# Kernel tuning notes

Hardware: AMD Instinct MI355X
Metric: run time of the kernel (lower is better)

## Reference

```python
import jax, jax.numpy as jnp
import numpy as np

M, B, S = 8, 64, 1024
I = K = V = 256
H = 8
F = 1024


def setup_inputs() -> dict:
    key0 = jax.random.key(0)
    ks = iter(jax.random.split(key0, 64))
    nrm = lambda shp, s=1.0: jax.random.normal(next(ks), shp, dtype=jnp.float32) * s
    w = 0.05
    inp = {
        's0': nrm((M, B, I)), 'q0': nrm((M, B, K)), 'k0': nrm((M, B, K)), 'v0': nrm((M, B, V)),
        'key': nrm((S, B, K)), 'value': nrm((S, B, V)),
        'attn_wq': nrm((M, K, K), w), 'attn_wk': nrm((M, K, K), w), 'attn_wv': nrm((M, K, K), w),
        'attn_bq': nrm((M, K), w), 'attn_bk': nrm((M, K), w), 'attn_bv': nrm((M, K), w),
        'attn_wo': nrm((M, K, K), w), 'attn_bo': nrm((M, K), w),
    }
    for p, out in (('q', K), ('k', K), ('v', V), ('s', I)):
        inp[p + '_w1'] = nrm((M, 2 * I, F), w)
        inp[p + '_b1'] = nrm((M, F), w)
        inp[p + '_w2'] = nrm((M, F, out), w)
        inp[p + '_b2'] = nrm((M, out), w)
    inp['g_w1'] = nrm((4, M, 2 * I, F), w)
    inp['g_b1'] = nrm((4, M, F), w)
    inp['g_w2'] = nrm((4, M, F, 1), w)
    inp['g_b2'] = nrm((4, M, 1), w)
    return inp


def _forward(s0, q0, k0, v0, key, value,
             attn_wq, attn_wk, attn_wv, attn_bq, attn_bk, attn_bv, attn_wo, attn_bo,
             q_w1, q_b1, q_w2, q_b2, k_w1, k_b1, k_w2, k_b2,
             v_w1, v_b1, v_w2, v_b2, s_w1, s_b1, s_w2, s_b2,
             g_w1, g_b1, g_w2, g_b2):
    m, b, kd = q0.shape
    s = key.shape[0]
    hd = kd // H
    # per-module projections (single-query decode-style attention)
    q = jnp.einsum('mbk,mkd->mbd', q0, attn_wq) + attn_bq[:, None, :]          # (M,B,K)
    kk = jnp.einsum('sbk,mkd->msbd', key, attn_wk) + attn_bk[:, None, None, :]  # (M,S,B,K)
    vv = jnp.einsum('sbk,mkd->msbd', value, attn_wv) + attn_bv[:, None, None, :]
    qh = q.reshape(m, b, H, hd)
    kh = kk.reshape(m, s, b, H, hd)
    vh = vv.reshape(m, s, b, H, hd)
    scores = jnp.einsum('mbhd,msbhd->mbhs', qh, kh) / jnp.sqrt(jnp.float32(hd))
    aw = jax.nn.softmax(scores, axis=-1)                                        # (M,B,H,S)
    ctx = jnp.einsum('mbhs,msbhd->mbhd', aw, vh).reshape(m, b, kd)
    attn_out = jnp.einsum('mbk,mko->mbo', ctx, attn_wo) + attn_bo[:, None, :]   # (M,B,K)
    attn_weights = aw.mean(axis=2)                                              # (M,B,S)

    # _make_mlp puts ReLU FIRST: Seq(ReLU, Lin, ReLU, Lin, last_act)
    fc_in = jax.nn.relu(jnp.concatenate([attn_out, s0], axis=-1))               # (M,B,2I)

    def head(w1, b1, w2, b2):
        h = jax.nn.relu(jnp.einsum('mbi,mif->mbf', fc_in, w1) + b1[:, None, :])
        return jnp.einsum('mbf,mfo->mbo', h, w2) + b2[:, None, :]

    # non-gate heads: last activation ReLU, then .tanh() in forward
    oq = jnp.tanh(jax.nn.relu(head(q_w1, q_b1, q_w2, q_b2)))
    ok = jnp.tanh(jax.nn.relu(head(k_w1, k_b1, k_w2, k_b2)))
    ov = jnp.tanh(jax.nn.relu(head(v_w1, v_b1, v_w2, v_b2)))
    os_ = jnp.tanh(jax.nn.relu(head(s_w1, s_b1, s_w2, s_b2)))

    # gate heads stacked on leading g axis (query,key,value,state)
    gh = jax.nn.relu(jnp.einsum('mbi,gmif->gmbf', fc_in, g_w1) + g_b1[:, :, None, :])
    gates = jax.nn.sigmoid(jnp.einsum('gmbf,gmfo->gmbo', gh, g_w2) + g_b2[:, :, None, :])
    qg, kg, vg, sg = gates[0], gates[1], gates[2], gates[3]

    gq = qg * oq + (1.0 - qg) * q0
    gk = kg * ok + (1.0 - kg) * k0
    gv = vg * ov + (1.0 - vg) * v0
    gs = sg * os_ + (1.0 - sg) * s0
    return attn_out, attn_weights, gs, gq, gk, gv


def reference(s0, q0, k0, v0, key, value,
              attn_wq, attn_wk, attn_wv, attn_bq, attn_bk, attn_bv, attn_wo, attn_bo,
              q_w1, q_b1, q_w2, q_b2, k_w1, k_b1, k_w2, k_b2,
              v_w1, v_b1, v_w2, v_b2, s_w1, s_b1, s_w2, s_b2,
              g_w1, g_b1, g_w2, g_b2):
    return _forward(s0, q0, k0, v0, key, value,
                    attn_wq, attn_wk, attn_wv, attn_bq, attn_bk, attn_bv, attn_wo, attn_bo,
                    q_w1, q_b1, q_w2, q_b2, k_w1, k_b1, k_w2, k_b2,
                    v_w1, v_b1, v_w2, v_b2, s_w1, s_b1, s_w2, s_b2,
                    g_w1, g_b1, g_w2, g_b2)
```

## Files before the change

kernel.cpp:

```cpp
#include <hip/hip_runtime.h>
#include <math.h>

#define Mm 8
#define Bb 64
#define Ss 1024
#define Kk 256
#define Hh 8
#define HD 32
#define Ff 1024

typedef _Float16 f16x8 __attribute__((ext_vector_type(8)));
typedef float f32x4 __attribute__((ext_vector_type(4)));

#define WS_Q      0u
#define WS_U      131072u
#define WS_QDB    1179648u
#define WS_SC     1183744u
#define WS_W      5378048u
#define WS_H1     6426624u
#define WS_FC     0u
#define WS_GATES  262144u
#define WS_HPART  1183744u

__device__ __forceinline__ unsigned pk2(float a, float b) {
  union { unsigned u; _Float16 h[2]; } c;
  c.h[0] = (_Float16)a; c.h[1] = (_Float16)b;
  return c.u;
}

__global__ __launch_bounds__(256) void k1_qproj(
    const float* __restrict__ q0, const float* __restrict__ wq,
    const float* __restrict__ bq, float* __restrict__ qout) {
  __shared__ float q0s[8 * 260];
  const int m = blockIdx.x, b0 = blockIdx.y * 8, t = threadIdx.x;
#pragma unroll
  for (int j = 0; j < 8; ++j)
    q0s[j * 260 + t] = q0[(m * Bb + b0 + j) * Kk + t];
  __syncthreads();
  float acc[8];
  const float bias = bq[m * Kk + t];
#pragma unroll
  for (int j = 0; j < 8; ++j) acc[j] = bias;
  const float* wcol = wq + m * Kk * Kk + t;
  for (int k4 = 0; k4 < Kk / 4; ++k4) {
    const float w0 = wcol[(k4 * 4 + 0) * Kk];
    const float w1 = wcol[(k4 * 4 + 1) * Kk];
    const float w2 = wcol[(k4 * 4 + 2) * Kk];
    const float w3 = wcol[(k4 * 4 + 3) * Kk];
#pragma unroll
    for (int j = 0; j < 8; ++j) {
      const float4 qv = *(const float4*)&q0s[j * 260 + k4 * 4];
      acc[j] += qv.x * w0 + qv.y * w1 + qv.z * w2 + qv.w * w3;
    }
  }
#pragma unroll
  for (int j = 0; j < 8; ++j)
    qout[(m * Bb + b0 + j) * Kk + t] = acc[j];
}

__global__ __launch_bounds__(256) void k2_uproj(
    const float* __restrict__ wk, const float* __restrict__ bk,
    const float* __restrict__ q, float* __restrict__ u,
    float* __restrict__ qdb) {
  __shared__ float qs[64 * 36];
  const int m = blockIdx.x, h = blockIdx.y, t = threadIdx.x;
#pragma unroll
  for (int p = 0; p < 8; ++p) {
    const int idx = p * 256 + t;
    const int d = idx & 31, b = idx >> 5;
    qs[b * 36 + d] = q[(m * Bb + b) * Kk + h * HD + d];
  }
  __syncthreads();
  float acc[64];
#pragma unroll
  for (int b = 0; b < 64; ++b) acc[b] = 0.f;
  const float* wrow = wk + (m * Kk + t) * Kk + h * HD;
#pragma unroll
  for (int d4 = 0; d4 < 8; ++d4) {
    const float4 w4 = *(const float4*)&wrow[d4 * 4];
#pragma unroll
    for (int b = 0; b < 64; ++b) {
      const float4 q4 = *(const float4*)&qs[b * 36 + d4 * 4];
      acc[b] += q4.x * w4.x + q4.y * w4.y + q4.z * w4.z + q4.w * w4.w;
    }
  }
  for (int b = 0; b < 64; ++b)
    u[((m * Bb + b) * Hh + h) * Kk + t] = acc[b];
  if (t < 64) {
    float s = 0.f;
#pragma unroll
    for (int d = 0; d < 32; ++d)
      s += qs[t * 36 + d] * bk[m * Kk + h * HD + d];
    qdb[(m * Bb + t) * Hh + h] = s;
  }
}

__global__ __launch_bounds__(256) void k3_scores(
    const float* __restrict__ key, const float* __restrict__ u,
    const float* __restrict__ qdb, float* __restrict__ sc) {
  __shared__ unsigned Us[2][64 * 20];
  __shared__ unsigned Ks[2][64 * 20];
  __shared__ float qd[64];
  const int b = blockIdx.x, st0 = blockIdx.y * 64, t = threadIdx.x;
  const int w = t >> 6, lane = t & 63, quad = lane >> 4, l15 = lane & 15;
  if (t < 64) qd[t] = qdb[((t >> 3) * Bb + b) * Hh + (t & 7)];
  const int umh = t >> 2, ukg = t & 3;
  const float* ug =
      u + (((umh >> 3) * Bb + b) * Hh + (umh & 7)) * Kk + ukg * 8;
  const int ksr = t >> 2, kkg = t & 3;
  const float* kg =
      key + (size_t)(st0 + ksr) * (Bb * Kk) + b * Kk + kkg * 8;
  float4 pu[2][2], pkv[2][2];
  f32x4 acc[4];
#pragma unroll
  for (int i = 0; i < 4; ++i) acc[i] = (f32x4){0.f, 0.f, 0.f, 0.f};

#define K3_LOAD(c, s)                                   \
  {                                                     \
    pu[s][0] = *(const float4*)(ug + (c) * 32);         \
    pu[s][1] = *(const float4*)(ug + (c) * 32 + 4);     \
    pkv[s][0] = *(const float4*)(kg + (c) * 32);        \
    pkv[s][1] = *(const float4*)(kg + (c) * 32 + 4);    \
  }
#define K3_STORE(buf, s)                                                   \
  {                                                                        \
    uint4 v;                                                               \
    v.x = pk2(pu[s][0].x, pu[s][0].y); v.y = pk2(pu[s][0].z, pu[s][0].w);  \
    v.z = pk2(pu[s][1].x, pu[s][1].y); v.w = pk2(pu[s][1].z, pu[s][1].w);  \
    *(uint4*)&Us[buf][umh * 20 + ukg * 4] = v;                             \
    uint4 q_;                                                              \
    q_.x = pk2(pkv[s][0].x, pkv[s][0].y);                                  \
    q_.y = pk2(pkv[s][0].z, pkv[s][0].w);                                  \
    q_.z = pk2(pkv[s][1].x, pkv[s][1].y);                                  \
    q_.w = pk2(pkv[s][1].z, pkv[s][1].w);                                  \
    *(uint4*)&Ks[buf][ksr * 20 + kkg * 4] = q_;                            \
  }

  K3_LOAD(0, 0); K3_STORE(0, 0);
  K3_LOAD(1, 1);
#pragma unroll
  for (int c = 0; c < 8; ++c) {
    __syncthreads();
    if (c + 2 < 8) K3_LOAD(c + 2, c & 1);
    const f16x8 af = *(const f16x8*)&Us[c & 1][(w * 16 + l15) * 20 + quad * 4];
#pragma unroll
    for (int sf = 0; sf < 4; ++sf) {
      const f16x8 bf =
          *(const f16x8*)&Ks[c & 1][(sf * 16 + l15) * 20 + quad * 4];
      acc[sf] =
          __builtin_amdgcn_mfma_f32_16x16x32_f16(af, bf, acc[sf], 0, 0, 0);
    }
    if (c + 1 < 8) K3_STORE((c + 1) & 1, (c + 1) & 1);
  }
  const float scale = 0.17677669529663687f;
#pragma unroll
  for (int sf = 0; sf < 4; ++sf) {
    const int s = st0 + sf * 16 + l15;
#pragma unroll
    for (int r = 0; r < 4; ++r) {
      const int mh = w * 16 + quad * 4 + r;
      sc[(size_t)(((mh >> 3) * Bb + b) * Hh + (mh & 7)) * Ss + s] =
          (acc[sf][r] + qd[mh]) * scale;
    }
  }
#undef K3_LOAD
#undef K3_STORE
}

__global__ __launch_bounds__(256) void k3b_softmax(float* __restrict__ sc) {
  __shared__ float red[8];
  const int row = blockIdx.x, t = threadIdx.x;
  const int lane = t & 63, wid = t >> 6;
  float4 v = *(const float4*)&sc[(size_t)row * 1024 + t * 4];
  float mx = fmaxf(fmaxf(v.x, v.y), fmaxf(v.z, v.w));
  for (int off = 32; off > 0; off >>= 1)
    mx = fmaxf(mx, __shfl_down(mx, off, 64));
  if (lane == 0) red[wid] = mx;
  __syncthreads();
  mx = fmaxf(fmaxf(red[0], red[1]), fmaxf(red[2], red[3]));
  v.x = __expf(v.x - mx); v.y = __expf(v.y - mx);
  v.z = __expf(v.z - mx); v.w = __expf(v.w - mx);
  float sm = v.x + v.y + v.z + v.w;
  for (int off = 32; off > 0; off >>= 1) sm += __shfl_down(sm, off, 64);
  if (lane == 0) red[4 + wid] = sm;
  __syncthreads();
  const float inv = 1.f / (red[4] + red[5] + red[6] + red[7]);
  v.x *= inv; v.y *= inv; v.z *= inv; v.w *= inv;
  *(float4*)&sc[(size_t)row * 1024 + t * 4] = v;
}

__global__ __launch_bounds__(256) void k3c_awmean(
    const float* __restrict__ sc, float* __restrict__ out) {
  const int m = blockIdx.x, b = blockIdx.y, t = threadIdx.x;
  const size_t base = (size_t)(m * Bb + b) * (Hh * Ss);
#pragma unroll
  for (int p = 0; p < 4; ++p) {
    const int s = p * 256 + t;
    float sum = 0.f;
#pragma unroll
    for (int h = 0; h < 8; ++h) sum += sc[base + h * 1024 + s];
    out[131072u + (m * Bb + b) * Ss + s] = sum * 0.125f;
  }
}

__global__ __launch_bounds__(256) void k4a_av(const float* __restrict__ value,
                                              const float* __restrict__ aw,
                                              float* __restrict__ wout) {
  __shared__ unsigned Ap[2][64 * 20];
  __shared__ unsigned Vp[2][32 * 20];
  const int b = blockIdx.x, ko = blockIdx.y, t = threadIdx.x;
  const int w = t >> 6, lane = t & 63, quad = lane >> 4, l15 = lane & 15;
  const int amh = t >> 2, asg = t & 3;
  const float* ag =
      aw + ((size_t)((amh >> 3) * Bb + b) * Hh + (amh & 7)) * Ss + asg * 8;
  const int vk = (t & 15) * 2, vsp = t >> 4;
  const float* vg = value + (size_t)(2 * vsp) * (Bb * Kk) + b * Kk +
                    ko * 32 + vk;
  const size_t srow = (size_t)(Bb * Kk);
  float4 pa[2][2];
  float2 pv[2][2];
  f32x4 acc[2];
  acc[0] = (f32x4){0.f, 0.f, 0.f, 0.f};
  acc[1] = (f32x4){0.f, 0.f, 0.f, 0.f};

#define K4_LOAD(c, s)                                         \
  {                                                           \
    pa[s][0] = *(const float4*)(ag + (c) * 32);               \
    pa[s][1] = *(const float4*)(ag + (c) * 32 + 4);           \
    const float* vb = vg + (size_t)(c) * 32 * srow;           \
    pv[s][0] = *(const float2*)vb;                            \
    pv[s][1] = *(const float2*)(vb + srow);                   \
  }
#define K4_STORE(buf, s)                                                   \
  {                                                                        \
    uint4 v;                                                               \
    v.x = pk2(pa[s][0].x, pa[s][0].y); v.y = pk2(pa[s][0].z, pa[s][0].w);  \
    v.z = pk2(pa[s][1].x, pa[s][1].y); v.w = pk2(pa[s][1].z, pa[s][1].w);  \
    *(uint4*)&Ap[buf][amh * 20 + asg * 4] = v;                             \
    Vp[buf][vk * 20 + vsp] = pk2(pv[s][0].x, pv[s][1].x);                  \
    Vp[buf][(vk + 1) * 20 + vsp] = pk2(pv[s][0].y, pv[s][1].y);            \
  }

  K4_LOAD(0, 0); K4_STORE(0, 0);
  K4_LOAD(1, 1);
#pragma unroll
  for (int c = 0; c < 32; ++c) {
    __syncthreads();
    if (c + 2 < 32) K4_LOAD(c + 2, c & 1);
    const f16x8 af = *(const f16x8*)&Ap[c & 1][(w * 16 + l15) * 20 + quad * 4];
#pragma unroll
    for (int nt = 0; nt < 2; ++nt) {
      const f16x8 bf =
          *(const f16x8*)&Vp[c & 1][(nt * 16 + l15) * 20 + quad * 4];
      acc[nt] =
          __builtin_amdgcn_mfma_f32_16x16x32_f16(af, bf, acc[nt], 0, 0, 0);
    }
    if (c + 1 < 32) K4_STORE((c + 1) & 1, (c + 1) & 1);
  }
#pragma unroll
  for (int nt = 0; nt < 2; ++nt) {
    const int k = ko * 32 + nt * 16 + l15;
#pragma unroll
    for (int r = 0; r < 4; ++r) {
      const int mh = w * 16 + quad * 4 + r;
      wout[((size_t)((mh >> 3) * Bb + b) * Hh + (mh & 7)) * Kk + k] =
          acc[nt][r];
    }
  }
#undef K4_LOAD
#undef K4_STORE
}

__global__ __launch_bounds__(256) void k5_ctx(
    const float* __restrict__ wv, const float* __restrict__ bv,
    const float* __restrict__ wo, const float* __restrict__ bo,
    const float* __restrict__ s0in, const float* __restrict__ w,
    float* __restrict__ attn_out, float* __restrict__ fc) {
  __shared__ float wsh[2048];
  __shared__ float ctxs[256];
  const int m = blockIdx.x, b = blockIdx.y, t = threadIdx.x;
  const int base = (m * Bb + b) * (Hh * Kk);
#pragma unroll
  for (int p = 0; p < 8; ++p) wsh[p * 256 + t] = w[base + p * 256 + t];
  __syncthreads();
  const int h = t >> 5;
  float acc = bv[m * Kk + t];
  const float* wvc = wv + m * Kk * Kk + t;
  for (int k4 = 0; k4 < 64; ++k4) {
    const float4 a4 = *(const float4*)&wsh[h * 256 + k4 * 4];
    acc += a4.x * wvc[(k4 * 4 + 0) * Kk] + a4.y * wvc[(k4 * 4 + 1) * Kk] +
           a4.z * wvc[(k4 * 4 + 2) * Kk] + a4.w * wvc[(k4 * 4 + 3) * Kk];
  }
  ctxs[t] = acc;
  __syncthreads();
  float acc2 = bo[m * Kk + t];
  const float* woc = wo + m * Kk * Kk + t;
  for (int k4 = 0; k4 < 64; ++k4) {
    const float4 c4 = *(const float4*)&ctxs[k4 * 4];
    acc2 += c4.x * woc[(k4 * 4 + 0) * Kk] + c4.y * woc[(k4 * 4 + 1) * Kk] +
            c4.z * woc[(k4 * 4 + 2) * Kk] + c4.w * woc[(k4 * 4 + 3) * Kk];
  }
  const int ob = (m * Bb + b) * Kk + t;
  attn_out[ob] = acc2;
  fc[(m * Bb + b) * 512 + t] = fmaxf(acc2, 0.f);
  fc[(m * Bb + b) * 512 + 256 + t] = fmaxf(s0in[ob], 0.f);
}

__global__ __launch_bounds__(256) void k6_mlp1(
    const float* __restrict__ fc, const float* __restrict__ w1q,
    const float* __restrict__ w1k, const float* __restrict__ w1v,
    const float* __restrict__ w1s, const float* __restrict__ w1g,
    const float* __restrict__ b1q, const float* __restrict__ b1k,
    const float* __restrict__ b1v, const float* __restrict__ b1s,
    const float* __restrict__ b1g, float* __restrict__ h1) {
  __shared__ unsigned As[2][64 * 20];
  __shared__ unsigned Ws[2][64 * 20];
  const int ft = blockIdx.x, m = blockIdx.y, head = blockIdx.z,
            t = threadIdx.x;
  const float* w1;
  const float* b1;
  if (head == 0)      { w1 = w1q; b1 = b1q; }
  else if (head == 1) { w1 = w1k; b1 = b1k; }
  else if (head == 2) { w1 = w1v; b1 = b1v; }
  else if (head == 3) { w1 = w1s; b1 = b1s; }
  else {
    w1 = w1g + (size_t)(head - 4) * (Mm * 512 * Ff);
    b1 = b1g + (head - 4) * (Mm * Ff);
  }
  w1 += (size_t)m * 512 * Ff;
  b1 += m * Ff;
  const int w = t >> 6, lane = t & 63, quad = lane >> 4, l15 = lane & 15;
  const int abb = t >> 2, akg = t & 3;
  const float* ag = fc + (m * Bb + abb) * 512 + akg * 8;
  const int wf0 = (t & 15) * 4, wkp = t >> 4;
  const float* wg = w1 + (size_t)(2 * wkp) * Ff + ft * 64 + wf0;
  float4 pa[2][2], pw[2][2];
  f32x4 acc[4];
#pragma unroll
  for (int i = 0; i < 4; ++i) acc[i] = (f32x4){0.f, 0.f, 0.f, 0.f};

#define K6_LOAD(c, s)                                            \
  {                                                              \
    pa[s][0] = *(const float4*)(ag + (c) * 32);                  \
    pa[s][1] = *(const float4*)(ag + (c) * 32 + 4);              \
    const float* wb = wg + (size_t)(c) * 32 * Ff;                \
    pw[s][0] = *(const float4*)wb;                               \
    pw[s][1] = *(const float4*)(wb + Ff);                        \
  }
#define K6_STORE(buf, s)                                                   \
  {                                                                        \
    uint4 v;                                                               \
    v.x = pk2(pa[s][0].x, pa[s][0].y); v.y = pk2(pa[s][0].z, pa[s][0].w);  \
    v.z = pk2(pa[s][1].x, pa[s][1].y); v.w = pk2(pa[s][1].z, pa[s][1].w);  \
    *(uint4*)&As[buf][abb * 20 + akg * 4] = v;                             \
    Ws[buf][(wf0 + 0) * 20 + wkp] = pk2(pw[s][0].x, pw[s][1].x);           \
    Ws[buf][(wf0 + 1) * 20 + wkp] = pk2(pw[s][0].y, pw[s][1].y);           \
    Ws[buf][(wf0 + 2) * 20 + wkp] = pk2(pw[s][0].z, pw[s][1].z);           \
    Ws[buf][(wf0 + 3) * 20 + wkp] = pk2(pw[s][0].w, pw[s][1].w);           \
  }

  K6_LOAD(0, 0); K6_STORE(0, 0);
  K6_LOAD(1, 1);
#pragma unroll
  for (int c = 0; c < 16; ++c) {
    __syncthreads();
    if (c + 2 < 16) K6_LOAD(c + 2, c & 1);
    const f16x8 bf = *(const f16x8*)&Ws[c & 1][(w * 16 + l15) * 20 + quad * 4];
#pragma unroll
    for (int mt = 0; mt < 4; ++mt) {
      const f16x8 af =
          *(const f16x8*)&As[c & 1][(mt * 16 + l15) * 20 + quad * 4];
      acc[mt] =
          __builtin_amdgcn_mfma_f32_16x16x32_f16(af, bf, acc[mt], 0, 0, 0);
    }
    if (c + 1 < 16) K6_STORE((c + 1) & 1, (c + 1) & 1);
  }
  const int f = ft * 64 + w * 16 + l15;
  const float bias = b1[f];
  float* hb = h1 + (size_t)((head * Mm + m) * Bb) * Ff + f;
#pragma unroll
  for (int mt = 0; mt < 4; ++mt) {
#pragma unroll
    for (int r = 0; r < 4; ++r) {
      const int bb = mt * 16 + quad * 4 + r;
      hb[(size_t)bb * Ff] = fmaxf(acc[mt][r] + bias, 0.f);
    }
  }
#undef K6_LOAD
#undef K6_STORE
}

__global__ __launch_bounds__(64) void k6b_gates(
    const float* __restrict__ h1, const float* __restrict__ gw2,
    const float* __restrict__ gb2, float* __restrict__ gates) {
  const int gm = blockIdx.x, b = blockIdx.y, t = threadIdx.x;
  const int g = gm >> 3, m = gm & 7;
  const float* hrow = h1 + (size_t)(((4 + g) * Mm + m) * Bb + b) * Ff;
  const float* wrow = gw2 + (g * Mm + m) * Ff;
  float s = 0.f;
#pragma unroll
  for (int i = 0; i < 16; ++i) s += hrow[t + i * 64] * wrow[t + i * 64];
  for (int off = 32; off > 0; off >>= 1) s += __shfl_down(s, off, 64);
  if (t == 0)
    gates[(g * Mm + m) * Bb + b] =
        1.f / (1.f + __expf(-(s + gb2[g * Mm + m])));
}

__global__ __launch_bounds__(256) void k7a_mlp2(
    const float* __restrict__ h1, const float* __restrict__ w2q,
    const float* __restrict__ w2k, const float* __restrict__ w2v,
    const float* __restrict__ w2s, float* __restrict__ hpart) {
  __shared__ float Ht[32 * 68];
  __shared__ float Wt[32 * 68];
  const int fq = blockIdx.x >> 2, oc = blockIdx.x & 3;
  const int m = blockIdx.y, head = blockIdx.z, t = threadIdx.x;
  const float* w2 =
      (head == 0) ? w2q : (head == 1) ? w2k : (head == 2) ? w2v : w2s;
  w2 += (size_t)m * Ff * Kk;
  const float* hbase = h1 + (size_t)((head * Mm + m) * Bb) * Ff + fq * 256;
  const int to = t & 15, tb = t >> 4;
  float acc[4][4];
#pragma unroll
  for (int j = 0; j < 4; ++j)
#pragma unroll
    for (int i = 0; i < 4; ++i) acc[j][i] = 0.f;
  for (int it = 0; it < 8; ++it) {
    __syncthreads();
#pragma unroll
    for (int p = 0; p < 8; ++p) {
      const int idx = p * 256 + t;
      const int f = idx & 31, bb = idx >> 5;
      Ht[f * 68 + bb] = hbase[bb * Ff + it * 32 + f];
    }
#pragma unroll
    for (int p = 0; p < 8; ++p) {
      const int idx = p * 256 + t;
      const int o = idx & 63, f = idx >> 6;
      Wt[f * 68 + o] = w2[(fq * 256 + it * 32 + f) * Kk + oc * 64 + o];
    }
    __syncthreads();
#pragma unroll 8
    for (int kk = 0; kk < 32; ++kk) {
      const float4 a4 = *(const float4*)&Ht[kk * 68 + tb * 4];
      const float4 w4 = *(const float4*)&Wt[kk * 68 + to * 4];
      acc[0][0] += a4.x * w4.x; acc[0][1] += a4.x * w4.y;
      acc[0][2] += a4.x * w4.z; acc[0][3] += a4.x * w4.w;
      acc[1][0] += a4.y * w4.x; acc[1][1] += a4.y * w4.y;
      acc[1][2] += a4.y * w4.z; acc[1][3] += a4.y * w4.w;
      acc[2][0] += a4.z * w4.x; acc[2][1] += a4.z * w4.y;
      acc[2][2] += a4.z * w4.z; acc[2][3] += a4.z * w4.w;
      acc[3][0] += a4.w * w4.x; acc[3][1] += a4.w * w4.y;
      acc[3][2] += a4.w * w4.z; acc[3][3] += a4.w * w4.w;
    }
  }
  float* hp =
      hpart + fq * 524288u + (size_t)((head * Mm + m) * Bb) * Kk + oc * 64;
#pragma unroll
  for (int j = 0; j < 4; ++j) {
    const int bb = tb * 4 + j;
    float4 r = {acc[j][0], acc[j][1], acc[j][2], acc[j][3]};
    *(float4*)&hp[bb * Kk + to * 4] = r;
  }
}

__global__ __launch_bounds__(256) void k7b_final(
    const float* __restrict__ hpart, const float* __restrict__ gates,
    const float* __restrict__ b2q, const float* __restrict__ b2k,
    const float* __restrict__ b2v, const float* __restrict__ b2s,
    const float* __restrict__ q0, const float* __restrict__ k0,
    const float* __restrict__ v0, const float* __restrict__ s0,
    float* __restrict__ out) {
  const int idx = blockIdx.x * 256 + threadIdx.x;
  const int o = idx & 255;
  const int b = (idx >> 8) & 63;
  const int m = (idx >> 14) & 7;
  const int head = idx >> 17;
  const float* b2 = (head == 0) ? b2q : (head == 1) ? b2k
                    : (head == 2) ? b2v : b2s;
  const float* x0 = (head == 0) ? q0 : (head == 1) ? k0
                    : (head == 2) ? v0 : s0;
  const unsigned ooff = (head == 0) ? 786432u
                        : (head == 1) ? 917504u
                        : (head == 2) ? 1048576u : 655360u;
  float v = hpart[idx] + hpart[524288u + idx] + hpart[1048576u + idx] +
            hpart[1572864u + idx] + b2[m * Kk + o];
  v = tanhf(fmaxf(v, 0.f));
  const float g = gates[(head * Mm + m) * Bb + b];
  const float x = x0[(m * Bb + b) * Kk + o];
  out[ooff + (m * Bb + b) * Kk + o] = g * v + (1.f - g) * x;
}

extern "C" void kernel_launch(void* const* d_in, const int* in_sizes, int n_in,
                              void* d_out, int out_size, void* d_ws,
                              size_t ws_size, hipStream_t stream) {
  (void)in_sizes; (void)n_in; (void)out_size; (void)ws_size;
  const float* s0  = (const float*)d_in[0];
  const float* q0  = (const float*)d_in[1];
  const float* k0  = (const float*)d_in[2];
  const float* v0  = (const float*)d_in[3];
  const float* key = (const float*)d_in[4];
  const float* val = (const float*)d_in[5];
  const float* wq  = (const float*)d_in[6];
  const float* wk  = (const float*)d_in[7];
  const float* wv  = (const float*)d_in[8];
  const float* bqa = (const float*)d_in[9];
  const float* bka = (const float*)d_in[10];
  const float* bva = (const float*)d_in[11];
  const float* wo  = (const float*)d_in[12];
  const float* bo  = (const float*)d_in[13];
  const float* qw1 = (const float*)d_in[14];
  const float* qb1 = (const float*)d_in[15];
  const float* qw2 = (const float*)d_in[16];
  const float* qb2 = (const float*)d_in[17];
  const float* kw1 = (const float*)d_in[18];
  const float* kb1 = (const float*)d_in[19];
  const float* kw2 = (const float*)d_in[20];
  const float* kb2 = (const float*)d_in[21];
  const float* vw1 = (const float*)d_in[22];
  const float* vb1 = (const float*)d_in[23];
  const float* vw2 = (const float*)d_in[24];
  const float* vb2 = (const float*)d_in[25];
  const float* sw1 = (const float*)d_in[26];
  const float* sb1 = (const float*)d_in[27];
  const float* sw2 = (const float*)d_in[28];
  const float* sb2 = (const float*)d_in[29];
  const float* gw1 = (const float*)d_in[30];
  const float* gb1 = (const float*)d_in[31];
  const float* gw2 = (const float*)d_in[32];
  const float* gb2 = (const float*)d_in[33];
  float* ws  = (float*)d_ws;
  float* out = (float*)d_out;

  k1_qproj<<<dim3(8, 8), 256, 0, stream>>>(q0, wq, bqa, ws + WS_Q);
  k2_uproj<<<dim3(8, 8), 256, 0, stream>>>(wk, bka, ws + WS_Q, ws + WS_U,
                                           ws + WS_QDB);
  k3_scores<<<dim3(64, 16), 256, 0, stream>>>(key, ws + WS_U, ws + WS_QDB,
                                              ws + WS_SC);
  k3b_softmax<<<dim3(4096), 256, 0, stream>>>(ws + WS_SC);
  k3c_awmean<<<dim3(8, 64), 256, 0, stream>>>(ws + WS_SC, out);
  k4a_av<<<dim3(64, 8), 256, 0, stream>>>(val, ws + WS_SC, ws + WS_W);
  k5_ctx<<<dim3(8, 64), 256, 0, stream>>>(wv, bva, wo, bo, s0, ws + WS_W, out,
                                          ws + WS_FC);
  k6_mlp1<<<dim3(16, 8, 8), 256, 0, stream>>>(ws + WS_FC, qw1, kw1, vw1, sw1,
                                              gw1, qb1, kb1, vb1, sb1, gb1,
                                              ws + WS_H1);
  k6b_gates<<<dim3(32, 64), 64, 0, stream>>>(ws + WS_H1, gw2, gb2,
                                             ws + WS_GATES);
  k7a_mlp2<<<dim3(16, 8, 4), 256, 0, stream>>>(ws + WS_H1, qw2, kw2, vw2, sw2,
                                               ws + WS_HPART);
  k7b_final<<<dim3(2048), 256, 0, stream>>>(ws + WS_HPART, ws + WS_GATES, qb2,
                                            kb2, vb2, sb2, q0, k0, v0, s0,
                                            out);
}
```

Before: 444.8 us.

## Fuse softmax with head-mean, vectorize W LDS stores, move MLP2 to MFMA

Softmax and the attention-weight head mean are merged into one kernel. Each block normalizes all 8 head rows for one (m,b) pair with wave-level shuffles, keeps them in LDS, and computes the mean there instead of re-reading scores from global memory. The k6 weight tile is stored transposed with uint4 LDS writes instead of scattered scalar stores. The fp32 SIMT k7 second-layer GEMM is replaced with a double-buffered fp16 MFMA path, which lowers precision on that GEMM. The fused softmax uses 32KB of LDS and launches 512 blocks instead of 4096, so there is less parallelism in that stage.

```diff
diff --git a/kernel.cpp b/kernel.cpp
--- a/kernel.cpp
+++ b/kernel.cpp
@@ -167,38 +167,61 @@
 #undef K3_STORE
 }
 
-__global__ __launch_bounds__(256) void k3b_softmax(float* __restrict__ sc) {
-  __shared__ float red[8];
-  const int row = blockIdx.x, t = threadIdx.x;
-  const int lane = t & 63, wid = t >> 6;
-  float4 v = *(const float4*)&sc[(size_t)row * 1024 + t * 4];
-  float mx = fmaxf(fmaxf(v.x, v.y), fmaxf(v.z, v.w));
-  for (int off = 32; off > 0; off >>= 1)
-    mx = fmaxf(mx, __shfl_down(mx, off, 64));
-  if (lane == 0) red[wid] = mx;
+__global__ __launch_bounds__(256) void k3b_softmax(float* __restrict__ sc,
+                                                   float* __restrict__ out) {
+  __shared__ float rows[8 * 1024];
+  const int m = blockIdx.x, b = blockIdx.y, t = threadIdx.x;
+  const int w = t >> 6, lane = t & 63;
+  const size_t base = (size_t)(m * Bb + b) * (Hh * Ss);
+#pragma unroll
+  for (int hh = 0; hh < 2; ++hh) {
+    const int h = w * 2 + hh;
+    float* g = sc + base + h * 1024;
+    float4 v0 = *(const float4*)&g[lane * 4];
+    float4 v1 = *(const float4*)&g[256 + lane * 4];
+    float4 v2 = *(const float4*)&g[512 + lane * 4];
+    float4 v3 = *(const float4*)&g[768 + lane * 4];
+    float mx = fmaxf(fmaxf(fmaxf(v0.x, v0.y), fmaxf(v0.z, v0.w)),
+                     fmaxf(fmaxf(v1.x, v1.y), fmaxf(v1.z, v1.w)));
+    mx = fmaxf(mx, fmaxf(fmaxf(fmaxf(v2.x, v2.y), fmaxf(v2.z, v2.w)),
+                         fmaxf(fmaxf(v3.x, v3.y), fmaxf(v3.z, v3.w))));
+#pragma unroll
+    for (int off = 32; off > 0; off >>= 1)
+      mx = fmaxf(mx, __shfl_xor(mx, off, 64));
+    v0.x = __expf(v0.x - mx); v0.y = __expf(v0.y - mx);
+    v0.z = __expf(v0.z - mx); v0.w = __expf(v0.w - mx);
+    v1.x = __expf(v1.x - mx); v1.y = __expf(v1.y - mx);
+    v1.z = __expf(v1.z - mx); v1.w = __expf(v1.w - mx);
+    v2.x = __expf(v2.x - mx); v2.y = __expf(v2.y - mx);
+    v2.z = __expf(v2.z - mx); v2.w = __expf(v2.w - mx);
+    v3.x = __expf(v3.x - mx); v3.y = __expf(v3.y - mx);
+    v3.z = __expf(v3.z - mx); v3.w = __expf(v3.w - mx);
+    float sm = v0.x + v0.y + v0.z + v0.w + v1.x + v1.y + v1.z + v1.w +
+               v2.x + v2.y + v2.z + v2.w + v3.x + v3.y + v3.z + v3.w;
+#pragma unroll
+    for (int off = 32; off > 0; off >>= 1) sm += __shfl_xor(sm, off, 64);
+    const float inv = 1.f / sm;
+    v0.x *= inv; v0.y *= inv; v0.z *= inv; v0.w *= inv;
+    v1.x *= inv; v1.y *= inv; v1.z *= inv; v1.w *= inv;
+    v2.x *= inv; v2.y *= inv; v2.z *= inv; v2.w *= inv;
+    v3.x *= inv; v3.y *= inv; v3.z *= inv; v3.w *= inv;
+    *(float4*)&g[lane * 4] = v0;
+    *(float4*)&g[256 + lane * 4] = v1;
+    *(float4*)&g[512 + lane * 4] = v2;
+    *(float4*)&g[768 + lane * 4] = v3;
+    float* r = rows + h * 1024;
+    *(float4*)&r[lane * 4] = v0;
+    *(float4*)&r[256 + lane * 4] = v1;
+    *(float4*)&r[512 + lane * 4] = v2;
+    *(float4*)&r[768 + lane * 4] = v3;
+  }
   __syncthreads();
-  mx = fmaxf(fmaxf(red[0], red[1]), fmaxf(red[2], red[3]));
-  v.x = __expf(v.x - mx); v.y = __expf(v.y - mx);
-  v.z = __expf(v.z - mx); v.w = __expf(v.w - mx);
-  float sm = v.x + v.y + v.z + v.w;
-  for (int off = 32; off > 0; off >>= 1) sm += __shfl_down(sm, off, 64);
-  if (lane == 0) red[4 + wid] = sm;
-  __syncthreads();
-  const float inv = 1.f / (red[4] + red[5] + red[6] + red[7]);
-  v.x *= inv; v.y *= inv; v.z *= inv; v.w *= inv;
-  *(float4*)&sc[(size_t)row * 1024 + t * 4] = v;
-}
-
-__global__ __launch_bounds__(256) void k3c_awmean(
-    const float* __restrict__ sc, float* __restrict__ out) {
-  const int m = blockIdx.x, b = blockIdx.y, t = threadIdx.x;
-  const size_t base = (size_t)(m * Bb + b) * (Hh * Ss);
 #pragma unroll
   for (int p = 0; p < 4; ++p) {
     const int s = p * 256 + t;
     float sum = 0.f;
 #pragma unroll
-    for (int h = 0; h < 8; ++h) sum += sc[base + h * 1024 + s];
+    for (int h = 0; h < 8; ++h) sum += rows[h * 1024 + s];
     out[131072u + (m * Bb + b) * Ss + s] = sum * 0.125f;
   }
 }
@@ -314,7 +337,7 @@
     const float* __restrict__ b1v, const float* __restrict__ b1s,
     const float* __restrict__ b1g, float* __restrict__ h1) {
   __shared__ unsigned As[2][64 * 20];
-  __shared__ unsigned Ws[2][64 * 20];
+  __shared__ unsigned Ws[2][16 * 68];
   const int ft = blockIdx.x, m = blockIdx.y, head = blockIdx.z,
             t = threadIdx.x;
   const float* w1;
@@ -353,10 +376,12 @@
     v.x = pk2(pa[s][0].x, pa[s][0].y); v.y = pk2(pa[s][0].z, pa[s][0].w);  \
     v.z = pk2(pa[s][1].x, pa[s][1].y); v.w = pk2(pa[s][1].z, pa[s][1].w);  \
     *(uint4*)&As[buf][abb * 20 + akg * 4] = v;                             \
-    Ws[buf][(wf0 + 0) * 20 + wkp] = pk2(pw[s][0].x, pw[s][1].x);           \
-    Ws[buf][(wf0 + 1) * 20 + wkp] = pk2(pw[s][0].y, pw[s][1].y);           \
-    Ws[buf][(wf0 + 2) * 20 + wkp] = pk2(pw[s][0].z, pw[s][1].z);           \
-    Ws[buf][(wf0 + 3) * 20 + wkp] = pk2(pw[s][0].w, pw[s][1].w);           \
+    uint4 wv_;                                                             \
+    wv_.x = pk2(pw[s][0].x, pw[s][1].x);                                   \
+    wv_.y = pk2(pw[s][0].y, pw[s][1].y);                                   \
+    wv_.z = pk2(pw[s][0].z, pw[s][1].z);                                   \
+    wv_.w = pk2(pw[s][0].w, pw[s][1].w);                                   \
+    *(uint4*)&Ws[buf][wkp * 68 + wf0] = wv_;                               \
   }
 
   K6_LOAD(0, 0); K6_STORE(0, 0);
@@ -365,7 +390,11 @@
   for (int c = 0; c < 16; ++c) {
     __syncthreads();
     if (c + 2 < 16) K6_LOAD(c + 2, c & 1);
-    const f16x8 bf = *(const f16x8*)&Ws[c & 1][(w * 16 + l15) * 20 + quad * 4];
+    union { f16x8 v; unsigned u[4]; } bfu;
+#pragma unroll
+    for (int j = 0; j < 4; ++j)
+      bfu.u[j] = Ws[c & 1][(quad * 4 + j) * 68 + w * 16 + l15];
+    const f16x8 bf = bfu.v;
 #pragma unroll
     for (int mt = 0; mt < 4; ++mt) {
       const f16x8 af =
@@ -410,57 +439,79 @@
     const float* __restrict__ h1, const float* __restrict__ w2q,
     const float* __restrict__ w2k, const float* __restrict__ w2v,
     const float* __restrict__ w2s, float* __restrict__ hpart) {
-  __shared__ float Ht[32 * 68];
-  __shared__ float Wt[32 * 68];
-  const int fq = blockIdx.x >> 2, oc = blockIdx.x & 3;
+  __shared__ unsigned As[2][64 * 20];
+  __shared__ unsigned Ws[2][16 * 68];
+  const int ot = blockIdx.x & 3, fq = blockIdx.x >> 2;
   const int m = blockIdx.y, head = blockIdx.z, t = threadIdx.x;
   const float* w2 =
       (head == 0) ? w2q : (head == 1) ? w2k : (head == 2) ? w2v : w2s;
   w2 += (size_t)m * Ff * Kk;
-  const float* hbase = h1 + (size_t)((head * Mm + m) * Bb) * Ff + fq * 256;
-  const int to = t & 15, tb = t >> 4;
-  float acc[4][4];
-#pragma unroll
-  for (int j = 0; j < 4; ++j)
-#pragma unroll
-    for (int i = 0; i < 4; ++i) acc[j][i] = 0.f;
-  for (int it = 0; it < 8; ++it) {
+  const int w = t >> 6, lane = t & 63, quad = lane >> 4, l15 = lane & 15;
+  const int abb = t >> 2, akg = t & 3;
+  const float* ag =
+      h1 + (size_t)((head * Mm + m) * Bb + abb) * Ff + fq * 256 + akg * 8;
+  const int wf0 = (t & 15) * 4, wkp = t >> 4;
+  const float* wg = w2 + (size_t)(fq * 256 + 2 * wkp) * Kk + ot * 64 + wf0;
+  float4 pa[2][2], pw[2][2];
+  f32x4 acc[4];
+#pragma unroll
+  for (int i = 0; i < 4; ++i) acc[i] = (f32x4){0.f, 0.f, 0.f, 0.f};
+
+#define K7_LOAD(c, s)                                            \
+  {                                                              \
+    pa[s][0] = *(const float4*)(ag + (c) * 32);                  \
+    pa[s][1] = *(const float4*)(ag + (c) * 32 + 4);              \
+    const float* wb = wg + (size_t)(c) * 32 * Kk;                \
+    pw[s][0] = *(const float4*)wb;                               \
+    pw[s][1] = *(const float4*)(wb + Kk);                        \
+  }
+#define K7_STORE(buf, s)                                                   \
+  {                                                                        \
+    uint4 v;                                                               \
+    v.x = pk2(pa[s][0].x, pa[s][0].y); v.y = pk2(pa[s][0].z, pa[s][0].w);  \
+    v.z = pk2(pa[s][1].x, pa[s][1].y); v.w = pk2(pa[s][1].z, pa[s][1].w);  \
+    *(uint4*)&As[buf][abb * 20 + akg * 4] = v;                             \
+    uint4 wv_;                                                             \
+    wv_.x = pk2(pw[s][0].x, pw[s][1].x);                                   \
+    wv_.y = pk2(pw[s][0].y, pw[s][1].y);                                   \
+    wv_.z = pk2(pw[s][0].z, pw[s][1].z);                                   \
+    wv_.w = pk2(pw[s][0].w, pw[s][1].w);                                   \
+    *(uint4*)&Ws[buf][wkp * 68 + wf0] = wv_;                               \
+  }
+
+  K7_LOAD(0, 0); K7_STORE(0, 0);
+  K7_LOAD(1, 1);
+#pragma unroll
+  for (int c = 0; c < 8; ++c) {
     __syncthreads();
-#pragma unroll
-    for (int p = 0; p < 8; ++p) {
-      const int idx = p * 256 + t;
-      const int f = idx & 31, bb = idx >> 5;
-      Ht[f * 68 + bb] = hbase[bb * Ff + it * 32 + f];
-    }
-#pragma unroll
-    for (int p = 0; p < 8; ++p) {
-      const int idx = p * 256 + t;
-      const int o = idx & 63, f = idx >> 6;
-      Wt[f * 68 + o] = w2[(fq * 256 + it * 32 + f) * Kk + oc * 64 + o];
-    }
-    __syncthreads();
-#pragma unroll 8
-    for (int kk = 0; kk < 32; ++kk) {
-      const float4 a4 = *(const float4*)&Ht[kk * 68 + tb * 4];
-      const float4 w4 = *(const float4*)&Wt[kk * 68 + to * 4];
-      acc[0][0] += a4.x * w4.x; acc[0][1] += a4.x * w4.y;
-      acc[0][2] += a4.x * w4.z; acc[0][3] += a4.x * w4.w;
-      acc[1][0] += a4.y * w4.x; acc[1][1] += a4.y * w4.y;
-      acc[1][2] += a4.y * w4.z; acc[1][3] += a4.y * w4.w;
-      acc[2][0] += a4.z * w4.x; acc[2][1] += a4.z * w4.y;
-      acc[2][2] += a4.z * w4.z; acc[2][3] += a4.z * w4.w;
-      acc[3][0] += a4.w * w4.x; acc[3][1] += a4.w * w4.y;
-      acc[3][2] += a4.w * w4.z; acc[3][3] += a4.w * w4.w;
-    }
-  }
+    if (c + 2 < 8) K7_LOAD(c + 2, c & 1);
+    union { f16x8 v; unsigned u[4]; } bfu;
+#pragma unroll
+    for (int j = 0; j < 4; ++j)
+      bfu.u[j] = Ws[c & 1][(quad * 4 + j) * 68 + w * 16 + l15];
+    const f16x8 bf = bfu.v;
+#pragma unroll
+    for (int mt = 0; mt < 4; ++mt) {
+      const f16x8 af =
+          *(const f16x8*)&As[c & 1][(mt * 16 + l15) * 20 + quad * 4];
+      acc[mt] =
+          __builtin_amdgcn_mfma_f32_16x16x32_f16(af, bf, acc[mt], 0, 0, 0);
+    }
+    if (c + 1 < 8) K7_STORE((c + 1) & 1, (c + 1) & 1);
+  }
+  const int o = ot * 64 + w * 16 + l15;
   float* hp =
-      hpart + fq * 524288u + (size_t)((head * Mm + m) * Bb) * Kk + oc * 64;
-#pragma unroll
-  for (int j = 0; j < 4; ++j) {
-    const int bb = tb * 4 + j;
-    float4 r = {acc[j][0], acc[j][1], acc[j][2], acc[j][3]};
-    *(float4*)&hp[bb * Kk + to * 4] = r;
-  }
+      hpart + fq * 524288u + (size_t)((head * Mm + m) * Bb) * Kk + o;
+#pragma unroll
+  for (int mt = 0; mt < 4; ++mt) {
+#pragma unroll
+    for (int r = 0; r < 4; ++r) {
+      const int bb = mt * 16 + quad * 4 + r;
+      hp[(size_t)bb * Kk] = acc[mt][r];
+    }
+  }
+#undef K7_LOAD
+#undef K7_STORE
 }
 
 __global__ __launch_bounds__(256) void k7b_final(
@@ -536,8 +587,7 @@
                                            ws + WS_QDB);
   k3_scores<<<dim3(64, 16), 256, 0, stream>>>(key, ws + WS_U, ws + WS_QDB,
                                               ws + WS_SC);
-  k3b_softmax<<<dim3(4096), 256, 0, stream>>>(ws + WS_SC);
-  k3c_awmean<<<dim3(8, 64), 256, 0, stream>>>(ws + WS_SC, out);
+  k3b_softmax<<<dim3(8, 64), 256, 0, stream>>>(ws + WS_SC, out);
   k4a_av<<<dim3(64, 8), 256, 0, stream>>>(val, ws + WS_SC, ws + WS_W);
   k5_ctx<<<dim3(8, 64), 256, 0, stream>>>(wv, bva, wo, bo, s0, ws + WS_W, out,
                                           ws + WS_FC);
```

After: 426.1 us. 4.2% less time.
